# Kernel tuning notes

Hardware: AMD Instinct MI355X
Metric: run time of the kernel (lower is better)

## Reference

```python
import jax, jax.numpy as jnp
import numpy as np

N_NODES = 50000
N_EDGES = 800000
IN_CH = 64
EDGE_DIM = 8
HIDDEN = 128
NUM_GRAPHS = 256


def setup_inputs() -> dict:
    key = jax.random.key(0)
    ks = jax.random.split(key, 16)
    x = jax.random.normal(ks[0], (N_NODES, IN_CH), dtype=jnp.float32)
    edge_index = jax.random.randint(ks[1], (2, N_EDGES), 0, N_NODES, dtype=jnp.int64)
    edge_attr = jax.random.normal(ks[2], (N_EDGES, EDGE_DIM), dtype=jnp.float32)
    batch = jnp.sort(jax.random.randint(ks[3], (N_NODES,), 0, NUM_GRAPHS, dtype=jnp.int64))

    def lin(k, fan_in, fan_out):
        bound = 1.0 / np.sqrt(fan_in)
        kw, kb = jax.random.split(k)
        W = jax.random.uniform(kw, (fan_in, fan_out), minval=-bound, maxval=bound, dtype=jnp.float32)
        b = jax.random.uniform(kb, (fan_out,), minval=-bound, maxval=bound, dtype=jnp.float32)
        return W, b

    W1, b1 = lin(ks[4], IN_CH, HIDDEN)
    We1, be1 = lin(ks[5], EDGE_DIM, IN_CH)
    W2, b2 = lin(ks[6], HIDDEN, HIDDEN)
    We2, be2 = lin(ks[7], EDGE_DIM, HIDDEN)
    W3, b3 = lin(ks[8], HIDDEN, HIDDEN)
    We3, be3 = lin(ks[9], EDGE_DIM, HIDDEN)
    return {"x": x, "edge_index": edge_index, "edge_attr": edge_attr, "batch": batch,
            "W1": W1, "b1": b1, "We1": We1, "be1": be1,
            "W2": W2, "b2": b2, "We2": We2, "be2": be2,
            "W3": W3, "b3": b3, "We3": We3, "be3": be3}


def gine_conv(x, src, dst, edge_attr, W, b, We, be):
    # edge feature projection to node-feature dim, then message = relu(x_j + e)
    e = edge_attr @ We + be                      # [E, d]
    msg = jax.nn.relu(x[src] + e)                # [E, d]
    agg = jax.ops.segment_sum(msg, dst, num_segments=x.shape[0])  # [N, d]
    # eps = 0 (PyG default, not trainable)
    return (x + agg) @ W + b


def reference(x, edge_index, edge_attr, batch,
              W1, b1, We1, be1, W2, b2, We2, be2, W3, b3, We3, be3):
    x = x.astype(jnp.float32)
    edge_attr = edge_attr.astype(jnp.float32)
    src, dst = edge_index[0], edge_index[1]
    x = jax.nn.relu(gine_conv(x, src, dst, edge_attr, W1, b1, We1, be1))
    x = jax.nn.relu(gine_conv(x, src, dst, edge_attr, W2, b2, We2, be2))
    x = jax.nn.relu(gine_conv(x, src, dst, edge_attr, W3, b3, We3, be3))
    # global mean pool over graphs
    sums = jax.ops.segment_sum(x, batch, num_segments=NUM_GRAPHS)          # [G, d]
    counts = jax.ops.segment_sum(jnp.ones((x.shape[0],), x.dtype), batch, num_segments=NUM_GRAPHS)
    return sums / jnp.maximum(counts, 1.0)[:, None]
```

## Files before the change

### kernel.cpp

```cpp
#include <hip/hip_runtime.h>
#include <hip/hip_bf16.h>
#include <hip/hip_fp16.h>

#define N_NODES 50000
#define N_EDGES 800000
#define IN_CH 64
#define EDGE_DIM 8
#define HIDDEN 128
#define NUM_GRAPHS 256
#define NPASS 2
#define PASS_W ((N_NODES + NPASS - 1) / NPASS)

typedef __attribute__((ext_vector_type(8))) _Float16 half8;
typedef __attribute__((ext_vector_type(4))) float floatx4;
typedef __attribute__((ext_vector_type(4))) int intx4;

static __device__ __forceinline__ __half2 u2h(int u) {
    union { int i; __half2 h; } cv; cv.i = u; return cv.h;
}
static __device__ __forceinline__ int h2u(__half2 h) {
    union { __half2 h; int i; } cv; cv.h = h; return cv.i;
}
static __device__ __forceinline__ unsigned short h1u(__half h) {
    union { __half h; unsigned short u; } cv; cv.h = h; return cv.u;
}

__global__ __launch_bounds__(256) void hist_kernel(
    const int* __restrict__ dst, int* __restrict__ deg, int E)
{
    int i = blockIdx.x * blockDim.x + threadIdx.x;
    if (i < E) atomicAdd(&deg[dst[i]], 1);
}

__global__ __launch_bounds__(256) void scan1_kernel(
    const int* __restrict__ deg, int* __restrict__ incl,
    int* __restrict__ blockSums, int N)
{
    __shared__ int s[256];
    int b = blockIdx.x, t = threadIdx.x;
    int i0 = b * 512 + 2 * t;
    int a0 = (i0 < N) ? deg[i0] : 0;
    int a1 = (i0 + 1 < N) ? deg[i0 + 1] : 0;
    int ps = a0 + a1;
    s[t] = ps;
    __syncthreads();
    for (int off = 1; off < 256; off <<= 1) {
        int v = (t >= off) ? s[t - off] : 0;
        __syncthreads();
        s[t] += v;
        __syncthreads();
    }
    int exclp = s[t] - ps;
    if (i0 < N)     incl[i0]     = exclp + a0;
    if (i0 + 1 < N) incl[i0 + 1] = exclp + a0 + a1;
    if (t == 255) blockSums[b] = s[255];
}

__global__ __launch_bounds__(128) void scan2_kernel(int* __restrict__ blockSums, int B)
{
    __shared__ int s[128];
    int t = threadIdx.x;
    int v = (t < B) ? blockSums[t] : 0;
    s[t] = v;
    __syncthreads();
    for (int off = 1; off < 128; off <<= 1) {
        int u = (t >= off) ? s[t - off] : 0;
        __syncthreads();
        s[t] += u;
        __syncthreads();
    }
    if (t < B) blockSums[t] = s[t] - v;
}

__global__ __launch_bounds__(256) void scan3_kernel(
    const int* __restrict__ incl, const int* __restrict__ deg,
    const int* __restrict__ blockSums, int* __restrict__ rowptr,
    int* __restrict__ pos, int N)
{
    int i = blockIdx.x * blockDim.x + threadIdx.x;
    if (i >= N) return;
    int v = incl[i] - deg[i] + blockSums[i >> 9];
    rowptr[i] = v;
    pos[i] = v;
}

__global__ __launch_bounds__(256) void scatter_pass_kernel(
    const int* __restrict__ dst, int* __restrict__ pos,
    int* __restrict__ eid, int lo, int E)
{
    int e = blockIdx.x * blockDim.x + threadIdx.x;
    if (e >= E) return;
    int d = dst[e];
    if ((unsigned)(d - lo) >= (unsigned)PASS_W) return;
    int p = atomicAdd(&pos[d], 1);
    eid[p] = e;
}

__global__ __launch_bounds__(256) void ranksort_gather_kernel(
    const int* __restrict__ eid, const int* __restrict__ src,
    const float* __restrict__ ea,
    const int* __restrict__ rowptr, const int* __restrict__ deg,
    int* __restrict__ src_s, __half* __restrict__ ea16, int N)
{
    int wave = threadIdx.x >> 6;
    int lane = threadIdx.x & 63;
    int n = blockIdx.x * 4 + wave;
    if (n >= N) return;
    int s = __builtin_amdgcn_readfirstlane(rowptr[n]);
    int d = __builtin_amdgcn_readfirstlane(deg[n]);

    for (int l = lane; l < d; l += 64) {
        int e = eid[s + l];
        int rank = 0;
        for (int i = 0; i < d; ++i)
            rank += (eid[s + i] < e) ? 1 : 0;
        int p = s + rank;
        src_s[p] = src[e];
        const float4* q = (const float4*)(ea + (size_t)e * EDGE_DIM);
        float4 a = q[0], b = q[1];
        __half2* o = (__half2*)(ea16 + (size_t)p * EDGE_DIM);
        o[0] = __floats2half2_rn(a.x, a.y);
        o[1] = __floats2half2_rn(a.z, a.w);
        o[2] = __floats2half2_rn(b.x, b.y);
        o[3] = __floats2half2_rn(b.z, b.w);
    }
}

#define XH_ELEMS (N_NODES * IN_CH)
__global__ __launch_bounds__(256) void cvt_all_kernel(
    const float* __restrict__ x, __half* __restrict__ xh,
    const float* __restrict__ W1, const float* __restrict__ W2,
    const float* __restrict__ W3,
    _Float16* __restrict__ Wt1, _Float16* __restrict__ Wt2,
    _Float16* __restrict__ Wt3)
{
    int idx = blockIdx.x * blockDim.x + threadIdx.x;
    if (idx < XH_ELEMS) { xh[idx] = __float2half(x[idx]); return; }
    idx -= XH_ELEMS;
    if (idx < 128 * IN_CH) {
        int n = idx / IN_CH, k = idx - n * IN_CH;
        Wt1[idx] = (_Float16)W1[k * 128 + n];
        return;
    }
    idx -= 128 * IN_CH;
    if (idx < 128 * HIDDEN) {
        int n = idx / HIDDEN, k = idx - n * HIDDEN;
        Wt2[idx] = (_Float16)W2[k * 128 + n];
        return;
    }
    idx -= 128 * HIDDEN;
    if (idx < 128 * HIDDEN) {
        int n = idx / HIDDEN, k = idx - n * HIDDEN;
        Wt3[idx] = (_Float16)W3[k * 128 + n];
    }
}

#define BF 8

__global__ __launch_bounds__(256) void gather_xs128_kernel(
    const __half* __restrict__ h,
    const int*    __restrict__ src_s,
    const __half* __restrict__ ea16,
    const int*    __restrict__ rowptr,
    const int*    __restrict__ deg,
    const float*  __restrict__ We,
    const float*  __restrict__ be,
    __half*       __restrict__ xs,
    int N)
{
    int wave = threadIdx.x >> 6;
    int n    = blockIdx.x * 4 + wave;
    if (n >= N) return;
    int l  = threadIdx.x & 63;
    int j0 = 2 * l;

    __half2 hw[8];
    #pragma unroll
    for (int k = 0; k < 8; ++k) {
        float2 wv = *(const float2*)&We[k * 128 + j0];
        hw[k] = __floats2half2_rn(wv.x, wv.y);
    }
    float2 bevf = *(const float2*)&be[j0];
    __half2 bev2 = __floats2half2_rn(bevf.x, bevf.y);

    int start = __builtin_amdgcn_readfirstlane(rowptr[n]);
    int dg    = __builtin_amdgcn_readfirstlane(deg[n]);

    float2 hf = __half22float2(*(const __half2*)&h[(size_t)n * 128 + j0]);
    float acc0 = hf.x, acc1 = hf.y;

    int nb = dg / BF;
    int base = start;
    for (int b = 0; b < nb; ++b, base += BF) {
        int sid[BF];
        #pragma unroll
        for (int t = 0; t < BF; ++t)
            sid[t] = __builtin_amdgcn_readfirstlane(
                __builtin_nontemporal_load(&src_s[base + t]));
        __half2 hraw[BF];
        #pragma unroll
        for (int t = 0; t < BF; ++t)
            hraw[t] = *(const __half2*)&h[(size_t)sid[t] * 128 + j0];
        intx4 eav[BF];
        #pragma unroll
        for (int t = 0; t < BF; ++t)
            eav[t] = __builtin_nontemporal_load(
                (const intx4*)&ea16[(size_t)(base + t) * 8]);

        #pragma unroll
        for (int t = 0; t < BF; ++t) {
            __half2 e01 = u2h(eav[t].x), e23 = u2h(eav[t].y);
            __half2 e45 = u2h(eav[t].z), e67 = u2h(eav[t].w);
            __half2 m = __hfma2(__low2half2(e01),  hw[0], bev2);
            m = __hfma2(__high2half2(e01), hw[1], m);
            m = __hfma2(__low2half2(e23),  hw[2], m);
            m = __hfma2(__high2half2(e23), hw[3], m);
            m = __hfma2(__low2half2(e45),  hw[4], m);
            m = __hfma2(__high2half2(e45), hw[5], m);
            m = __hfma2(__low2half2(e67),  hw[6], m);
            m = __hfma2(__high2half2(e67), hw[7], m);
            m = __hadd2(m, hraw[t]);
            float2 mf = __half22float2(m);
            acc0 += mf.x > 0.0f ? mf.x : 0.0f;
            acc1 += mf.y > 0.0f ? mf.y : 0.0f;
        }
    }
    int end = start + dg;
    for (int idx = base; idx < end; ++idx) {
        int s = __builtin_amdgcn_readfirstlane(src_s[idx]);
        __half2 hr = *(const __half2*)&h[(size_t)s * 128 + j0];
        intx4 ev = __builtin_nontemporal_load((const intx4*)&ea16[(size_t)idx * 8]);
        __half2 e01 = u2h(ev.x), e23 = u2h(ev.y), e45 = u2h(ev.z), e67 = u2h(ev.w);
        __half2 m = __hfma2(__low2half2(e01),  hw[0], bev2);
        m = __hfma2(__high2half2(e01), hw[1], m);
        m = __hfma2(__low2half2(e23),  hw[2], m);
        m = __hfma2(__high2half2(e23), hw[3], m);
        m = __hfma2(__low2half2(e45),  hw[4], m);
        m = __hfma2(__high2half2(e45), hw[5], m);
        m = __hfma2(__low2half2(e67),  hw[6], m);
        m = __hfma2(__high2half2(e67), hw[7], m);
        m = __hadd2(m, hr);
        float2 mf = __half22float2(m);
        acc0 += mf.x > 0.0f ? mf.x : 0.0f;
        acc1 += mf.y > 0.0f ? mf.y : 0.0f;
    }
    __builtin_nontemporal_store(h2u(__floats2half2_rn(acc0, acc1)),
                                (int*)&xs[(size_t)n * 128 + j0]);
}

__global__ __launch_bounds__(256) void gather_xs64_kernel(
    const __half* __restrict__ h,
    const int*    __restrict__ src_s,
    const __half* __restrict__ ea16,
    const int*    __restrict__ rowptr,
    const int*    __restrict__ deg,
    const float*  __restrict__ We,
    const float*  __restrict__ be,
    __half*       __restrict__ xs,
    int N)
{
    int wave = threadIdx.x >> 6;
    int n    = blockIdx.x * 4 + wave;
    if (n >= N) return;
    int j = threadIdx.x & 63;

    __half2 w2[4];
    #pragma unroll
    for (int p = 0; p < 4; ++p)
        w2[p] = __floats2half2_rn(We[(2 * p) * 64 + j], We[(2 * p + 1) * 64 + j]);
    float bej = be[j];

    int start = __builtin_amdgcn_readfirstlane(rowptr[n]);
    int dg    = __builtin_amdgcn_readfirstlane(deg[n]);

    float acc = __half2float(h[(size_t)n * 64 + j]);

    int nb = dg / BF;
    int base = start;
    for (int b = 0; b < nb; ++b, base += BF) {
        int sid[BF];
        #pragma unroll
        for (int t = 0; t < BF; ++t)
            sid[t] = __builtin_amdgcn_readfirstlane(
                __builtin_nontemporal_load(&src_s[base + t]));
        __half hraw[BF];
        #pragma unroll
        for (int t = 0; t < BF; ++t)
            hraw[t] = h[(size_t)sid[t] * 64 + j];
        intx4 eav[BF];
        #pragma unroll
        for (int t = 0; t < BF; ++t)
            eav[t] = __builtin_nontemporal_load(
                (const intx4*)&ea16[(size_t)(base + t) * 8]);

        #pragma unroll
        for (int t = 0; t < BF; ++t) {
            __half2 d = __hmul2(u2h(eav[t].x), w2[0]);
            d = __hfma2(u2h(eav[t].y), w2[1], d);
            d = __hfma2(u2h(eav[t].z), w2[2], d);
            d = __hfma2(u2h(eav[t].w), w2[3], d);
            float proj = __half2float(__low2half(d)) + __half2float(__high2half(d));
            float m = __half2float(hraw[t]) + proj + bej;
            acc += m > 0.0f ? m : 0.0f;
        }
    }
    int end = start + dg;
    for (int idx = base; idx < end; ++idx) {
        int s = __builtin_amdgcn_readfirstlane(src_s[idx]);
        __half hr = h[(size_t)s * 64 + j];
        intx4 ev = __builtin_nontemporal_load((const intx4*)&ea16[(size_t)idx * 8]);
        __half2 d = __hmul2(u2h(ev.x), w2[0]);
        d = __hfma2(u2h(ev.y), w2[1], d);
        d = __hfma2(u2h(ev.z), w2[2], d);
        d = __hfma2(u2h(ev.w), w2[3], d);
        float proj = __half2float(__low2half(d)) + __half2float(__high2half(d));
        float m = __half2float(hr) + proj + bej;
        acc += m > 0.0f ? m : 0.0f;
    }
    __builtin_nontemporal_store(h1u(__float2half(acc)),
                                (unsigned short*)&xs[(size_t)n * 64 + j]);
}

template<int K>
__global__ __launch_bounds__(256) void node_mfma_kernel(
    const _Float16* __restrict__ xs,
    const _Float16* __restrict__ Wt,
    const float*    __restrict__ b,
    _Float16*       __restrict__ out,
    int N)
{
    int wave  = threadIdx.x >> 6;
    int lane  = threadIdx.x & 63;
    int row16 = lane & 15;
    int quad  = lane >> 4;
    int m0    = (blockIdx.x * 4 + wave) * 32;

    int nA = m0 + row16;        if (nA >= N) nA = N - 1;
    int nB = m0 + 16 + row16;   if (nB >= N) nB = N - 1;

    floatx4 accA[8], accB[8];
    #pragma unroll
    for (int t = 0; t < 8; ++t) { accA[t] = (floatx4)(0.0f); accB[t] = (floatx4)(0.0f); }

    #pragma unroll
    for (int kc = 0; kc < K; kc += 32) {
        half8 a0 = __builtin_nontemporal_load((const half8*)&xs[(size_t)nA * K + kc + quad * 8]);
        half8 a1 = __builtin_nontemporal_load((const half8*)&xs[(size_t)nB * K + kc + quad * 8]);
        #pragma unroll
        for (int t = 0; t < 8; ++t) {
            half8 bf = *(const half8*)&Wt[(size_t)(t * 16 + row16) * K + kc + quad * 8];
            accA[t] = __builtin_amdgcn_mfma_f32_16x16x32_f16(a0, bf, accA[t], 0, 0, 0);
            accB[t] = __builtin_amdgcn_mfma_f32_16x16x32_f16(a1, bf, accB[t], 0, 0, 0);
        }
    }

    #pragma unroll
    for (int t = 0; t < 8; ++t) {
        int col = t * 16 + row16;
        float bj = b[col];
        #pragma unroll
        for (int r = 0; r < 4; ++r) {
            int nodeA = m0 + quad * 4 + r;
            if (nodeA < N) {
                float v = accA[t][r] + bj;
                out[(size_t)nodeA * 128 + col] = (_Float16)(v > 0.0f ? v : 0.0f);
            }
            int nodeB = m0 + 16 + quad * 4 + r;
            if (nodeB < N) {
                float v = accB[t][r] + bj;
                out[(size_t)nodeB * 128 + col] = (_Float16)(v > 0.0f ? v : 0.0f);
            }
        }
    }
}

__global__ __launch_bounds__(128) void pool_kernel(
    const __half* __restrict__ h,
    const int*    __restrict__ batch,
    float*        __restrict__ out,
    int N)
{
    __shared__ int s_lo, s_hi;
    int g = blockIdx.x;
    int j = threadIdx.x;

    if (j == 0) {
        int lo = 0, hi = N;
        while (lo < hi) { int m = (lo + hi) >> 1; if (batch[m] < g) lo = m + 1; else hi = m; }
        s_lo = lo;
        int lo2 = lo, hi2 = N;
        while (lo2 < hi2) { int m = (lo2 + hi2) >> 1; if (batch[m] < g + 1) lo2 = m + 1; else hi2 = m; }
        s_hi = lo2;
    }
    __syncthreads();

    int lo = s_lo, hi = s_hi;
    float acc = 0.0f;
    #pragma unroll 4
    for (int n = lo; n < hi; ++n) {
        acc += __half2float(h[(size_t)n * HIDDEN + j]);
    }
    float c = (float)(hi - lo);
    out[g * HIDDEN + j] = acc / (c > 1.0f ? c : 1.0f);
}

extern "C" void kernel_launch(void* const* d_in, const int* in_sizes, int n_in,
                              void* d_out, int out_size, void* d_ws, size_t ws_size,
                              hipStream_t stream)
{
    const float* x   = (const float*)d_in[0];
    const int*   ei  = (const int*)d_in[1];
    const float* ea  = (const float*)d_in[2];
    const int*   bat = (const int*)d_in[3];
    const float* W1  = (const float*)d_in[4];
    const float* b1  = (const float*)d_in[5];
    const float* We1 = (const float*)d_in[6];
    const float* be1 = (const float*)d_in[7];
    const float* W2  = (const float*)d_in[8];
    const float* b2  = (const float*)d_in[9];
    const float* We2 = (const float*)d_in[10];
    const float* be2 = (const float*)d_in[11];
    const float* W3  = (const float*)d_in[12];
    const float* b3  = (const float*)d_in[13];
    const float* We3 = (const float*)d_in[14];
    const float* be3 = (const float*)d_in[15];
    float* out = (float*)d_out;

    const int* src = ei;
    const int* dst = ei + N_EDGES;

    int* deg       = (int*)d_ws;
    int* rowptr    = deg + N_NODES;
    int* pos       = rowptr + N_NODES;
    int* eid       = pos + N_NODES;
    int* src_s     = eid + N_EDGES;
    int* blockSums = src_s + N_EDGES;
    __half* ea16   = (__half*)(blockSums + 128);
    __half* xs     = ea16 + (size_t)N_EDGES * EDGE_DIM;
    __half* xh     = xs + (size_t)N_NODES * HIDDEN;
    __half* h1h    = xh + (size_t)N_NODES * IN_CH;
    __half* h2h    = h1h + (size_t)N_NODES * HIDDEN;
    _Float16* Wt1  = (_Float16*)(h2h + (size_t)N_NODES * HIDDEN);
    _Float16* Wt2  = Wt1 + 128 * IN_CH;
    _Float16* Wt3  = Wt2 + 128 * HIDDEN;

    const int BLK = 256;
    const int NB_E = (N_EDGES + BLK - 1) / BLK;
    const int NB_N = (N_NODES + BLK - 1) / BLK;
    const int SCAN_B = (N_NODES + 511) / 512;
    const int MFMA_B = (N_NODES + 127) / 128;
    const int WAVE4_B = (N_NODES + 3) / 4;
    const int CVT_ELEMS = XH_ELEMS + 128 * IN_CH + 2 * 128 * HIDDEN;

    (void)hipMemsetAsync(deg, 0, N_NODES * sizeof(int), stream);
    hist_kernel<<<NB_E, BLK, 0, stream>>>(dst, deg, N_EDGES);
    scan1_kernel<<<SCAN_B, 256, 0, stream>>>(deg, pos, blockSums, N_NODES);
    scan2_kernel<<<1, 128, 0, stream>>>(blockSums, SCAN_B);
    scan3_kernel<<<NB_N, BLK, 0, stream>>>(pos, deg, blockSums, rowptr, pos, N_NODES);
    for (int pass = 0; pass < NPASS; ++pass) {
        scatter_pass_kernel<<<NB_E, BLK, 0, stream>>>(
            dst, pos, eid, pass * PASS_W, N_EDGES);
    }
    ranksort_gather_kernel<<<WAVE4_B, BLK, 0, stream>>>(
        eid, src, ea, rowptr, deg, src_s, ea16, N_NODES);
    cvt_all_kernel<<<(CVT_ELEMS + BLK - 1) / BLK, BLK, 0, stream>>>(
        x, xh, W1, W2, W3, Wt1, Wt2, Wt3);

    gather_xs64_kernel<<<WAVE4_B, BLK, 0, stream>>>(
        xh, src_s, ea16, rowptr, deg, We1, be1, xs, N_NODES);
    node_mfma_kernel<IN_CH><<<MFMA_B, 256, 0, stream>>>(
        (const _Float16*)xs, Wt1, b1, (_Float16*)h1h, N_NODES);

    gather_xs128_kernel<<<WAVE4_B, BLK, 0, stream>>>(
        h1h, src_s, ea16, rowptr, deg, We2, be2, xs, N_NODES);
    node_mfma_kernel<HIDDEN><<<MFMA_B, 256, 0, stream>>>(
        (const _Float16*)xs, Wt2, b2, (_Float16*)h2h, N_NODES);

    gather_xs128_kernel<<<WAVE4_B, BLK, 0, stream>>>(
        h2h, src_s, ea16, rowptr, deg, We3, be3, xs, N_NODES);
    node_mfma_kernel<HIDDEN><<<MFMA_B, 256, 0, stream>>>(
        (const _Float16*)xs, Wt3, b3, (_Float16*)h1h, N_NODES);

    pool_kernel<<<NUM_GRAPHS, 128, 0, stream>>>(h1h, bat, out, N_NODES);
}
```

Before: 428.6 us.

## Software-pipeline edge gathers with lane-broadcast indices and register rank sort

The gather kernels now load up to 64 source indices at once with one coalesced vector load and broadcast them with readlane. Edge batches are double-buffered so the next batch's row and edge-attribute loads are in flight while the current batch is computed, with the remainder handled by clamped, predicated batches. The rank-sort kernel now ranks nodes of degree at most 64 by comparing register values through readlane instead of rereading eid from memory for every comparison. The intent is to cut scalar load latency and serialized memory round-trips in these latency-bound gathers, at the cost of more register pressure and some redundant clamped loads.

```diff
diff --git a/kernel.cpp b/kernel.cpp
--- a/kernel.cpp
+++ b/kernel.cpp
@@ -109,20 +109,40 @@
     int s = __builtin_amdgcn_readfirstlane(rowptr[n]);
     int d = __builtin_amdgcn_readfirstlane(deg[n]);
 
-    for (int l = lane; l < d; l += 64) {
-        int e = eid[s + l];
+    if (d <= 64) {
+        int e = (lane < d) ? eid[s + lane] : 0x7fffffff;
         int rank = 0;
-        for (int i = 0; i < d; ++i)
-            rank += (eid[s + i] < e) ? 1 : 0;
-        int p = s + rank;
-        src_s[p] = src[e];
-        const float4* q = (const float4*)(ea + (size_t)e * EDGE_DIM);
-        float4 a = q[0], b = q[1];
-        __half2* o = (__half2*)(ea16 + (size_t)p * EDGE_DIM);
-        o[0] = __floats2half2_rn(a.x, a.y);
-        o[1] = __floats2half2_rn(a.z, a.w);
-        o[2] = __floats2half2_rn(b.x, b.y);
-        o[3] = __floats2half2_rn(b.z, b.w);
+        for (int i = 0; i < d; ++i) {
+            int v = __builtin_amdgcn_readlane(e, i);
+            rank += (v < e) ? 1 : 0;
+        }
+        if (lane < d) {
+            int p = s + rank;
+            src_s[p] = src[e];
+            const float4* q = (const float4*)(ea + (size_t)e * EDGE_DIM);
+            float4 a = q[0], b = q[1];
+            __half2* o = (__half2*)(ea16 + (size_t)p * EDGE_DIM);
+            o[0] = __floats2half2_rn(a.x, a.y);
+            o[1] = __floats2half2_rn(a.z, a.w);
+            o[2] = __floats2half2_rn(b.x, b.y);
+            o[3] = __floats2half2_rn(b.z, b.w);
+        }
+    } else {
+        for (int l = lane; l < d; l += 64) {
+            int e = eid[s + l];
+            int rank = 0;
+            for (int i = 0; i < d; ++i)
+                rank += (eid[s + i] < e) ? 1 : 0;
+            int p = s + rank;
+            src_s[p] = src[e];
+            const float4* q = (const float4*)(ea + (size_t)e * EDGE_DIM);
+            float4 a = q[0], b = q[1];
+            __half2* o = (__half2*)(ea16 + (size_t)p * EDGE_DIM);
+            o[0] = __floats2half2_rn(a.x, a.y);
+            o[1] = __floats2half2_rn(a.z, a.w);
+            o[2] = __floats2half2_rn(b.x, b.y);
+            o[3] = __floats2half2_rn(b.z, b.w);
+        }
     }
 }
 
@@ -189,60 +209,60 @@
     float2 hf = __half22float2(*(const __half2*)&h[(size_t)n * 128 + j0]);
     float acc0 = hf.x, acc1 = hf.y;
 
-    int nb = dg / BF;
-    int base = start;
-    for (int b = 0; b < nb; ++b, base += BF) {
-        int sid[BF];
-        #pragma unroll
-        for (int t = 0; t < BF; ++t)
-            sid[t] = __builtin_amdgcn_readfirstlane(
-                __builtin_nontemporal_load(&src_s[base + t]));
-        __half2 hraw[BF];
-        #pragma unroll
-        for (int t = 0; t < BF; ++t)
-            hraw[t] = *(const __half2*)&h[(size_t)sid[t] * 128 + j0];
-        intx4 eav[BF];
-        #pragma unroll
-        for (int t = 0; t < BF; ++t)
-            eav[t] = __builtin_nontemporal_load(
-                (const intx4*)&ea16[(size_t)(base + t) * 8]);
-
-        #pragma unroll
-        for (int t = 0; t < BF; ++t) {
-            __half2 e01 = u2h(eav[t].x), e23 = u2h(eav[t].y);
-            __half2 e45 = u2h(eav[t].z), e67 = u2h(eav[t].w);
-            __half2 m = __hfma2(__low2half2(e01),  hw[0], bev2);
-            m = __hfma2(__high2half2(e01), hw[1], m);
-            m = __hfma2(__low2half2(e23),  hw[2], m);
-            m = __hfma2(__high2half2(e23), hw[3], m);
-            m = __hfma2(__low2half2(e45),  hw[4], m);
-            m = __hfma2(__high2half2(e45), hw[5], m);
-            m = __hfma2(__low2half2(e67),  hw[6], m);
-            m = __hfma2(__high2half2(e67), hw[7], m);
-            m = __hadd2(m, hraw[t]);
-            float2 mf = __half22float2(m);
-            acc0 += mf.x > 0.0f ? mf.x : 0.0f;
-            acc1 += mf.y > 0.0f ? mf.y : 0.0f;
-        }
-    }
-    int end = start + dg;
-    for (int idx = base; idx < end; ++idx) {
-        int s = __builtin_amdgcn_readfirstlane(src_s[idx]);
-        __half2 hr = *(const __half2*)&h[(size_t)s * 128 + j0];
-        intx4 ev = __builtin_nontemporal_load((const intx4*)&ea16[(size_t)idx * 8]);
-        __half2 e01 = u2h(ev.x), e23 = u2h(ev.y), e45 = u2h(ev.z), e67 = u2h(ev.w);
-        __half2 m = __hfma2(__low2half2(e01),  hw[0], bev2);
-        m = __hfma2(__high2half2(e01), hw[1], m);
-        m = __hfma2(__low2half2(e23),  hw[2], m);
-        m = __hfma2(__high2half2(e23), hw[3], m);
-        m = __hfma2(__low2half2(e45),  hw[4], m);
-        m = __hfma2(__high2half2(e45), hw[5], m);
-        m = __hfma2(__low2half2(e67),  hw[6], m);
-        m = __hfma2(__high2half2(e67), hw[7], m);
-        m = __hadd2(m, hr);
-        float2 mf = __half22float2(m);
-        acc0 += mf.x > 0.0f ? mf.x : 0.0f;
-        acc1 += mf.y > 0.0f ? mf.y : 0.0f;
+    for (int c = 0; c < dg; c += 64) {
+        int rem = dg - c; if (rem > 64) rem = 64;
+        int idx = c + l; if (idx > dg - 1) idx = dg - 1;
+        int sidv = __builtin_nontemporal_load(&src_s[start + idx]);
+
+        int nbt = (rem + BF - 1) / BF;
+
+        __half2 hrA[BF]; intx4 evA[BF];
+        __half2 hrB[BF]; intx4 evB[BF];
+
+        auto ISSUE = [&](int b0, __half2* hr, intx4* ev) {
+            int cnt = rem - b0; if (cnt > BF) cnt = BF;
+            #pragma unroll
+            for (int t = 0; t < BF; ++t) {
+                int tt = t < cnt ? t : cnt - 1;
+                int sid = __builtin_amdgcn_readlane(sidv, b0 + tt);
+                hr[t] = *(const __half2*)&h[(size_t)sid * 128 + j0];
+                ev[t] = __builtin_nontemporal_load(
+                    (const intx4*)&ea16[(size_t)(start + c + b0 + tt) * 8]);
+            }
+        };
+        auto COMPUTE = [&](int b0, __half2* hr, intx4* ev) {
+            int cnt = rem - b0; if (cnt > BF) cnt = BF;
+            #pragma unroll
+            for (int t = 0; t < BF; ++t) {
+                if (t < cnt) {
+                    __half2 e01 = u2h(ev[t].x), e23 = u2h(ev[t].y);
+                    __half2 e45 = u2h(ev[t].z), e67 = u2h(ev[t].w);
+                    __half2 m = __hfma2(__low2half2(e01),  hw[0], bev2);
+                    m = __hfma2(__high2half2(e01), hw[1], m);
+                    m = __hfma2(__low2half2(e23),  hw[2], m);
+                    m = __hfma2(__high2half2(e23), hw[3], m);
+                    m = __hfma2(__low2half2(e45),  hw[4], m);
+                    m = __hfma2(__high2half2(e45), hw[5], m);
+                    m = __hfma2(__low2half2(e67),  hw[6], m);
+                    m = __hfma2(__high2half2(e67), hw[7], m);
+                    m = __hadd2(m, hr[t]);
+                    float2 mf = __half22float2(m);
+                    acc0 += mf.x > 0.0f ? mf.x : 0.0f;
+                    acc1 += mf.y > 0.0f ? mf.y : 0.0f;
+                }
+            }
+        };
+
+        ISSUE(0, hrA, evA);
+        int b = 0;
+        while (true) {
+            if (b + 1 < nbt) ISSUE((b + 1) * BF, hrB, evB);
+            COMPUTE(b * BF, hrA, evA);
+            if (++b >= nbt) break;
+            if (b + 1 < nbt) ISSUE((b + 1) * BF, hrA, evA);
+            COMPUTE(b * BF, hrB, evB);
+            if (++b >= nbt) break;
+        }
     }
     __builtin_nontemporal_store(h2u(__floats2half2_rn(acc0, acc1)),
                                 (int*)&xs[(size_t)n * 128 + j0]);
@@ -275,47 +295,53 @@
 
     float acc = __half2float(h[(size_t)n * 64 + j]);
 
-    int nb = dg / BF;
-    int base = start;
-    for (int b = 0; b < nb; ++b, base += BF) {
-        int sid[BF];
-        #pragma unroll
-        for (int t = 0; t < BF; ++t)
-            sid[t] = __builtin_amdgcn_readfirstlane(
-                __builtin_nontemporal_load(&src_s[base + t]));
-        __half hraw[BF];
-        #pragma unroll
-        for (int t = 0; t < BF; ++t)
-            hraw[t] = h[(size_t)sid[t] * 64 + j];
-        intx4 eav[BF];
-        #pragma unroll
-        for (int t = 0; t < BF; ++t)
-            eav[t] = __builtin_nontemporal_load(
-                (const intx4*)&ea16[(size_t)(base + t) * 8]);
-
-        #pragma unroll
-        for (int t = 0; t < BF; ++t) {
-            __half2 d = __hmul2(u2h(eav[t].x), w2[0]);
-            d = __hfma2(u2h(eav[t].y), w2[1], d);
-            d = __hfma2(u2h(eav[t].z), w2[2], d);
-            d = __hfma2(u2h(eav[t].w), w2[3], d);
-            float proj = __half2float(__low2half(d)) + __half2float(__high2half(d));
-            float m = __half2float(hraw[t]) + proj + bej;
-            acc += m > 0.0f ? m : 0.0f;
-        }
-    }
-    int end = start + dg;
-    for (int idx = base; idx < end; ++idx) {
-        int s = __builtin_amdgcn_readfirstlane(src_s[idx]);
-        __half hr = h[(size_t)s * 64 + j];
-        intx4 ev = __builtin_nontemporal_load((const intx4*)&ea16[(size_t)idx * 8]);
-        __half2 d = __hmul2(u2h(ev.x), w2[0]);
-        d = __hfma2(u2h(ev.y), w2[1], d);
-        d = __hfma2(u2h(ev.z), w2[2], d);
-        d = __hfma2(u2h(ev.w), w2[3], d);
-        float proj = __half2float(__low2half(d)) + __half2float(__high2half(d));
-        float m = __half2float(hr) + proj + bej;
-        acc += m > 0.0f ? m : 0.0f;
+    for (int c = 0; c < dg; c += 64) {
+        int rem = dg - c; if (rem > 64) rem = 64;
+        int idx = c + j; if (idx > dg - 1) idx = dg - 1;
+        int sidv = __builtin_nontemporal_load(&src_s[start + idx]);
+
+        int nbt = (rem + BF - 1) / BF;
+
+        __half hrA[BF]; intx4 evA[BF];
+        __half hrB[BF]; intx4 evB[BF];
+
+        auto ISSUE = [&](int b0, __half* hr, intx4* ev) {
+            int cnt = rem - b0; if (cnt > BF) cnt = BF;
+            #pragma unroll
+            for (int t = 0; t < BF; ++t) {
+                int tt = t < cnt ? t : cnt - 1;
+                int sid = __builtin_amdgcn_readlane(sidv, b0 + tt);
+                hr[t] = h[(size_t)sid * 64 + j];
+                ev[t] = __builtin_nontemporal_load(
+                    (const intx4*)&ea16[(size_t)(start + c + b0 + tt) * 8]);
+            }
+        };
+        auto COMPUTE = [&](int b0, __half* hr, intx4* ev) {
+            int cnt = rem - b0; if (cnt > BF) cnt = BF;
+            #pragma unroll
+            for (int t = 0; t < BF; ++t) {
+                if (t < cnt) {
+                    __half2 d = __hmul2(u2h(ev[t].x), w2[0]);
+                    d = __hfma2(u2h(ev[t].y), w2[1], d);
+                    d = __hfma2(u2h(ev[t].z), w2[2], d);
+                    d = __hfma2(u2h(ev[t].w), w2[3], d);
+                    float proj = __half2float(__low2half(d)) + __half2float(__high2half(d));
+                    float m = __half2float(hr[t]) + proj + bej;
+                    acc += m > 0.0f ? m : 0.0f;
+                }
+            }
+        };
+
+        ISSUE(0, hrA, evA);
+        int b = 0;
+        while (true) {
+            if (b + 1 < nbt) ISSUE((b + 1) * BF, hrB, evB);
+            COMPUTE(b * BF, hrA, evA);
+            if (++b >= nbt) break;
+            if (b + 1 < nbt) ISSUE((b + 1) * BF, hrA, evA);
+            COMPUTE(b * BF, hrB, evB);
+            if (++b >= nbt) break;
+        }
     }
     __builtin_nontemporal_store(h1u(__float2half(acc)),
                                 (unsigned short*)&xs[(size_t)n * 64 + j]);
```

Result: no change. 437.0 us (+1.9%).

## Split 128-wide edge gather into feature slices and use register rank sort

Applied to the files above, without the earlier changes.

The 128-channel gather now runs as four launches, each covering a 32-channel slice. In each launch a wave handles four edges at once: 16 lanes per edge, with the source ids broadcast by shuffle and partial sums combined by a cross-lane reduction. The intent is to shrink each pass's gathered working set so it stays in cache and to get more memory requests in flight per wave. The cost is reading the edge attributes and source ids four times and extra launches. Separately, the rank sort for nodes with degree up to 64 now compares edge ids held in registers via readlane instead of re-reading global memory.

```diff
diff --git a/kernel.cpp b/kernel.cpp
--- a/kernel.cpp
+++ b/kernel.cpp
@@ -109,20 +109,40 @@
     int s = __builtin_amdgcn_readfirstlane(rowptr[n]);
     int d = __builtin_amdgcn_readfirstlane(deg[n]);
 
-    for (int l = lane; l < d; l += 64) {
-        int e = eid[s + l];
+    if (d <= 64) {
+        int e = (lane < d) ? eid[s + lane] : 0x7fffffff;
         int rank = 0;
-        for (int i = 0; i < d; ++i)
-            rank += (eid[s + i] < e) ? 1 : 0;
-        int p = s + rank;
-        src_s[p] = src[e];
-        const float4* q = (const float4*)(ea + (size_t)e * EDGE_DIM);
-        float4 a = q[0], b = q[1];
-        __half2* o = (__half2*)(ea16 + (size_t)p * EDGE_DIM);
-        o[0] = __floats2half2_rn(a.x, a.y);
-        o[1] = __floats2half2_rn(a.z, a.w);
-        o[2] = __floats2half2_rn(b.x, b.y);
-        o[3] = __floats2half2_rn(b.z, b.w);
+        for (int i = 0; i < d; ++i) {
+            int v = __builtin_amdgcn_readlane(e, i);
+            rank += (v < e) ? 1 : 0;
+        }
+        if (lane < d) {
+            int p = s + rank;
+            src_s[p] = src[e];
+            const float4* q = (const float4*)(ea + (size_t)e * EDGE_DIM);
+            float4 a = q[0], b = q[1];
+            __half2* o = (__half2*)(ea16 + (size_t)p * EDGE_DIM);
+            o[0] = __floats2half2_rn(a.x, a.y);
+            o[1] = __floats2half2_rn(a.z, a.w);
+            o[2] = __floats2half2_rn(b.x, b.y);
+            o[3] = __floats2half2_rn(b.z, b.w);
+        }
+    } else {
+        for (int l = lane; l < d; l += 64) {
+            int e = eid[s + l];
+            int rank = 0;
+            for (int i = 0; i < d; ++i)
+                rank += (eid[s + i] < e) ? 1 : 0;
+            int p = s + rank;
+            src_s[p] = src[e];
+            const float4* q = (const float4*)(ea + (size_t)e * EDGE_DIM);
+            float4 a = q[0], b = q[1];
+            __half2* o = (__half2*)(ea16 + (size_t)p * EDGE_DIM);
+            o[0] = __floats2half2_rn(a.x, a.y);
+            o[1] = __floats2half2_rn(a.z, a.w);
+            o[2] = __floats2half2_rn(b.x, b.y);
+            o[3] = __floats2half2_rn(b.z, b.w);
+        }
     }
 }
 
@@ -155,9 +175,10 @@
     }
 }
 
-#define BF 8
-
-__global__ __launch_bounds__(256) void gather_xs128_kernel(
+#define GS 4
+#define UD 6
+
+__global__ __launch_bounds__(256) void gather128_slice_kernel(
     const __half* __restrict__ h,
     const int*    __restrict__ src_s,
     const __half* __restrict__ ea16,
@@ -166,13 +187,15 @@
     const float*  __restrict__ We,
     const float*  __restrict__ be,
     __half*       __restrict__ xs,
-    int N)
+    int N, int s)
 {
     int wave = threadIdx.x >> 6;
     int n    = blockIdx.x * 4 + wave;
     if (n >= N) return;
-    int l  = threadIdx.x & 63;
-    int j0 = 2 * l;
+    int l    = threadIdx.x & 63;
+    int egrp = l >> 4;
+    int fl   = l & 15;
+    int j0   = (s << 5) + 2 * fl;
 
     __half2 hw[8];
     #pragma unroll
@@ -187,66 +210,62 @@
     int dg    = __builtin_amdgcn_readfirstlane(deg[n]);
 
     float2 hf = __half22float2(*(const __half2*)&h[(size_t)n * 128 + j0]);
-    float acc0 = hf.x, acc1 = hf.y;
-
-    int nb = dg / BF;
-    int base = start;
-    for (int b = 0; b < nb; ++b, base += BF) {
-        int sid[BF];
-        #pragma unroll
-        for (int t = 0; t < BF; ++t)
-            sid[t] = __builtin_amdgcn_readfirstlane(
-                __builtin_nontemporal_load(&src_s[base + t]));
-        __half2 hraw[BF];
-        #pragma unroll
-        for (int t = 0; t < BF; ++t)
-            hraw[t] = *(const __half2*)&h[(size_t)sid[t] * 128 + j0];
-        intx4 eav[BF];
-        #pragma unroll
-        for (int t = 0; t < BF; ++t)
-            eav[t] = __builtin_nontemporal_load(
-                (const intx4*)&ea16[(size_t)(base + t) * 8]);
-
-        #pragma unroll
-        for (int t = 0; t < BF; ++t) {
-            __half2 e01 = u2h(eav[t].x), e23 = u2h(eav[t].y);
-            __half2 e45 = u2h(eav[t].z), e67 = u2h(eav[t].w);
-            __half2 m = __hfma2(__low2half2(e01),  hw[0], bev2);
-            m = __hfma2(__high2half2(e01), hw[1], m);
-            m = __hfma2(__low2half2(e23),  hw[2], m);
-            m = __hfma2(__high2half2(e23), hw[3], m);
-            m = __hfma2(__low2half2(e45),  hw[4], m);
-            m = __hfma2(__high2half2(e45), hw[5], m);
-            m = __hfma2(__low2half2(e67),  hw[6], m);
-            m = __hfma2(__high2half2(e67), hw[7], m);
-            m = __hadd2(m, hraw[t]);
-            float2 mf = __half22float2(m);
-            acc0 += mf.x > 0.0f ? mf.x : 0.0f;
-            acc1 += mf.y > 0.0f ? mf.y : 0.0f;
-        }
-    }
-    int end = start + dg;
-    for (int idx = base; idx < end; ++idx) {
-        int s = __builtin_amdgcn_readfirstlane(src_s[idx]);
-        __half2 hr = *(const __half2*)&h[(size_t)s * 128 + j0];
-        intx4 ev = __builtin_nontemporal_load((const intx4*)&ea16[(size_t)idx * 8]);
-        __half2 e01 = u2h(ev.x), e23 = u2h(ev.y), e45 = u2h(ev.z), e67 = u2h(ev.w);
-        __half2 m = __hfma2(__low2half2(e01),  hw[0], bev2);
-        m = __hfma2(__high2half2(e01), hw[1], m);
-        m = __hfma2(__low2half2(e23),  hw[2], m);
-        m = __hfma2(__high2half2(e23), hw[3], m);
-        m = __hfma2(__low2half2(e45),  hw[4], m);
-        m = __hfma2(__high2half2(e45), hw[5], m);
-        m = __hfma2(__low2half2(e67),  hw[6], m);
-        m = __hfma2(__high2half2(e67), hw[7], m);
-        m = __hadd2(m, hr);
-        float2 mf = __half22float2(m);
-        acc0 += mf.x > 0.0f ? mf.x : 0.0f;
-        acc1 += mf.y > 0.0f ? mf.y : 0.0f;
-    }
-    __builtin_nontemporal_store(h2u(__floats2half2_rn(acc0, acc1)),
-                                (int*)&xs[(size_t)n * 128 + j0]);
-}
+    float acc0 = (egrp == 0) ? hf.x : 0.0f;
+    float acc1 = (egrp == 0) ? hf.y : 0.0f;
+
+    for (int c = 0; c < dg; c += 64) {
+        int rem = dg - c; if (rem > 64) rem = 64;
+        int idx = c + l; if (idx > dg - 1) idx = dg - 1;
+        int sidv = __builtin_nontemporal_load(&src_s[start + idx]);
+        int cbase = start + c;
+
+        int ng = (rem + 3) >> 2;
+        for (int g0 = 0; g0 < ng; g0 += UD) {
+            int gcnt = ng - g0; if (gcnt > UD) gcnt = UD;
+            __half2 hrS[UD]; intx4 evS[UD];
+            #pragma unroll
+            for (int t = 0; t < UD; ++t) {
+                int g  = g0 + (t < gcnt ? t : gcnt - 1);
+                int e4 = 4 * g + egrp;
+                int ec = (e4 < rem) ? e4 : rem - 1;
+                int sid = __shfl(sidv, ec);
+                hrS[t] = *(const __half2*)&h[(size_t)sid * 128 + j0];
+                evS[t] = __builtin_nontemporal_load(
+                    (const intx4*)&ea16[(size_t)(cbase + ec) * 8]);
+            }
+            #pragma unroll
+            for (int t = 0; t < UD; ++t) {
+                if (t < gcnt) {
+                    int e4 = 4 * (g0 + t) + egrp;
+                    __half2 e01 = u2h(evS[t].x), e23 = u2h(evS[t].y);
+                    __half2 e45 = u2h(evS[t].z), e67 = u2h(evS[t].w);
+                    __half2 m = __hfma2(__low2half2(e01),  hw[0], bev2);
+                    m = __hfma2(__high2half2(e01), hw[1], m);
+                    m = __hfma2(__low2half2(e23),  hw[2], m);
+                    m = __hfma2(__high2half2(e23), hw[3], m);
+                    m = __hfma2(__low2half2(e45),  hw[4], m);
+                    m = __hfma2(__high2half2(e45), hw[5], m);
+                    m = __hfma2(__low2half2(e67),  hw[6], m);
+                    m = __hfma2(__high2half2(e67), hw[7], m);
+                    m = __hadd2(m, hrS[t]);
+                    float2 mf = __half22float2(m);
+                    if (e4 < rem) {
+                        acc0 += mf.x > 0.0f ? mf.x : 0.0f;
+                        acc1 += mf.y > 0.0f ? mf.y : 0.0f;
+                    }
+                }
+            }
+        }
+    }
+
+    acc0 += __shfl_xor(acc0, 16); acc1 += __shfl_xor(acc1, 16);
+    acc0 += __shfl_xor(acc0, 32); acc1 += __shfl_xor(acc1, 32);
+    if (egrp == 0)
+        __builtin_nontemporal_store(h2u(__floats2half2_rn(acc0, acc1)),
+                                    (int*)&xs[(size_t)n * 128 + j0]);
+}
+
+#define BF 8
 
 __global__ __launch_bounds__(256) void gather_xs64_kernel(
     const __half* __restrict__ h,
@@ -471,13 +490,15 @@
     node_mfma_kernel<IN_CH><<<MFMA_B, 256, 0, stream>>>(
         (const _Float16*)xs, Wt1, b1, (_Float16*)h1h, N_NODES);
 
-    gather_xs128_kernel<<<WAVE4_B, BLK, 0, stream>>>(
-        h1h, src_s, ea16, rowptr, deg, We2, be2, xs, N_NODES);
+    for (int s = 0; s < GS; ++s)
+        gather128_slice_kernel<<<WAVE4_B, BLK, 0, stream>>>(
+            h1h, src_s, ea16, rowptr, deg, We2, be2, xs, N_NODES, s);
     node_mfma_kernel<HIDDEN><<<MFMA_B, 256, 0, stream>>>(
         (const _Float16*)xs, Wt2, b2, (_Float16*)h2h, N_NODES);
 
-    gather_xs128_kernel<<<WAVE4_B, BLK, 0, stream>>>(
-        h2h, src_s, ea16, rowptr, deg, We3, be3, xs, N_NODES);
+    for (int s = 0; s < GS; ++s)
+        gather128_slice_kernel<<<WAVE4_B, BLK, 0, stream>>>(
+            h2h, src_s, ea16, rowptr, deg, We3, be3, xs, N_NODES, s);
     node_mfma_kernel<HIDDEN><<<MFMA_B, 256, 0, stream>>>(
         (const _Float16*)xs, Wt3, b3, (_Float16*)h1h, N_NODES);
 
```

Result: slower. 616.6 us (+43.9%).
